# Performance work log

Measured on AMD Instinct MI355X. Metric: run time of the kernel, lower is better.

## Reference

```python
import jax, jax.numpy as jnp
import numpy as np

B, S, H = 64, 512, 768
A1, C1 = 100, 300          # token-attention and sentence-classifier hidden sizes
BETA = 1.0                 # soft_attention_beta
SLW, TLW, RLW = 1.0, 1.0, 0.01  # loss weights


def setup_inputs() -> dict:
    key = jax.random.key(0)
    ks = jax.random.split(key, 12)
    hidden_states = jax.random.normal(ks[0], (B, S, H), jnp.float32)
    # token_attention: Linear(H,100) -> Tanh -> Linear(100,1) -> Sigmoid
    w1 = jax.random.normal(ks[1], (H, A1), jnp.float32) * 0.02
    b1 = jnp.zeros((A1,), jnp.float32)
    w2 = jax.random.normal(ks[2], (A1, 1), jnp.float32) * 0.02
    b2 = jnp.zeros((1,), jnp.float32)
    # sentence_classification: Linear(H,300) -> Tanh -> Linear(300,1) -> Sigmoid
    sw1 = jax.random.normal(ks[3], (H, C1), jnp.float32) * 0.02
    sb1 = jnp.zeros((C1,), jnp.float32)
    sw2 = jax.random.normal(ks[4], (C1, 1), jnp.float32) * 0.02
    sb2 = jnp.zeros((1,), jnp.float32)
    offset_mapping = jax.random.randint(ks[5], (B, S, 2), 0, 4).astype(jnp.int32)
    offset_mapping = offset_mapping.at[:, 0, 0].set(0)  # first token starts a word
    # labels in {-1, 0, 1}; -1 = ignore
    labels = jax.random.randint(ks[6], (B, S), -1, 2).astype(jnp.float32)
    return {
        "hidden_states": hidden_states,
        "w1": w1, "b1": b1, "w2": w2, "b2": b2,
        "sw1": sw1, "sb1": sb1, "sw2": sw2, "sb2": sb2,
        "labels": labels,
        "offset_mapping": offset_mapping,
    }


def _forward(hidden_states, w1, b1, w2, b2, sw1, sb1, sw2, sb2, labels, offset_mapping):
    # token attention scores in (0,1): [B, S]
    token_att = jax.nn.sigmoid(
        jnp.tanh(hidden_states @ w1 + b1) @ w2 + b2
    )[..., 0]

    # ragged per-word subword max-pooling (segment-max along the sequence)
    not_subword = offset_mapping[:, :, 0] == 0                 # [B, S] word starts
    seg = jnp.maximum(jnp.cumsum(not_subword.astype(jnp.int32), axis=1) - 1, 0)

    def _seg_max(vals, seg_ids):
        return jax.ops.segment_max(vals, seg_ids, num_segments=S)

    segmax = jax.vmap(_seg_max)(token_att, seg)                # [B, S] per-word max
    word_att = jnp.where(not_subword, jnp.take_along_axis(segmax, seg, axis=1), 0.0)

    # mask: labeled tokens that are word starts
    token_mask = ((labels != -1) & not_subword).astype(token_att.dtype)
    masked = word_att * token_mask                              # token_logits [B, S]

    # beta-normalized soft attention pooling over hidden states
    p = masked ** BETA
    att_norm = p / jnp.sum(p, axis=1, keepdims=True)            # [B, S]
    pooled = jnp.einsum("bsh,bs->bh", hidden_states, att_norm)  # [B, H]

    sent = jax.nn.sigmoid(jnp.tanh(pooled @ sw1 + sb1) @ sw2 + sb2)  # [B, 1]

    # losses (MSE with reduction='sum')
    sentence_labels = jnp.max(labels, axis=1, keepdims=True)    # [B, 1]
    sentence_loss = jnp.sum((sent - sentence_labels) ** 2)
    zero_labels = jnp.where(labels != -1, labels, 0.0)
    token_loss = jnp.sum((masked - zero_labels) ** 2)
    ones_masked = jnp.where(masked == 0, 1.0, masked)
    reg_a = jnp.sum(jnp.min(ones_masked, axis=1, keepdims=True) ** 2)
    reg_b = jnp.sum((jnp.max(masked, axis=1, keepdims=True) - sentence_labels) ** 2)
    total = SLW * sentence_loss + TLW * token_loss + RLW * (reg_a + reg_b)
    return total, sentence_loss, token_loss, reg_a, reg_b, masked, sent


def reference(hidden_states, w1, b1, w2, b2, sw1, sb1, sw2, sb2, labels, offset_mapping):
    return _forward(hidden_states, w1, b1, w2, b2, sw1, sb1, sw2, sb2,
                    labels, offset_mapping)
```

## Files before the change

### kernel.cpp

```cpp
#include <hip/hip_runtime.h>
#include <math.h>

#define BB 64
#define SS 512
#define HH 768
#define AA1 100
#define CC1 300

typedef __bf16 bf16x8 __attribute__((ext_vector_type(8)));
typedef float f32x4 __attribute__((ext_vector_type(4)));

#ifndef __has_builtin
#define __has_builtin(x) 0
#endif
#if __has_builtin(__builtin_amdgcn_global_load_lds)
#define HAVE_GLL 1
#else
#define HAVE_GLL 0
#endif

#define AS1 __attribute__((address_space(1)))
#define AS3 __attribute__((address_space(3)))

__global__ __launch_bounds__(256) void k_prep(const float* __restrict__ w1,
                                              __bf16* __restrict__ w1i) {
    int idx = blockIdx.x * 256 + threadIdx.x;
    int j = idx % 112;
    int r = idx / 112;
    int e = r & 7, g = r >> 3;
    int k = (g >> 2) * 32 + (g & 3) * 8 + e;
    float v = (j < AA1) ? w1[k * AA1 + j] : 0.f;
    w1i[((size_t)g * 112 + j) * 8 + e] = (__bf16)v;
}

__global__ __launch_bounds__(256) void k_token_att(
        const float* __restrict__ hs, const __bf16* __restrict__ w1i,
        const float* __restrict__ b1, const float* __restrict__ w2,
        const float* __restrict__ b2, float* __restrict__ token_att) {
    __shared__ __attribute__((aligned(16))) float lA[4096];
    __shared__ __attribute__((aligned(16))) __bf16 lB[3584];

    const int tid = threadIdx.x;
    const int tok0 = blockIdx.x * 128;
    const int w = tid >> 6, lane = tid & 63;
    const int q = lane >> 4, ln = lane & 15;
    const int t0 = w * 32 + ln;
    const int t1 = t0 + 16;

    f32x4 acc0[7], acc1[7];
#pragma unroll
    for (int n = 0; n < 7; n++) {
        acc0[n] = (f32x4){0.f, 0.f, 0.f, 0.f};
        acc1[n] = (f32x4){0.f, 0.f, 0.f, 0.f};
    }

    const int p0 = (2 * q) ^ (ln & 7);
    const int p1 = (2 * q + 1) ^ (ln & 7);

    for (int kt = 0; kt < 24; kt++) {
        const int ko = kt * 32;
#pragma unroll
        for (int it = 0; it < 4; it++) {
            int i = tid + it * 256;
            int tt = i >> 3, c = (i & 7) ^ (tt & 7);
            const float* g = hs + (size_t)(tok0 + tt) * HH + ko + c * 4;
#if HAVE_GLL
            __builtin_amdgcn_global_load_lds((AS1 void*)g,
                    (AS3 void*)(lA + (it * 256 + w * 64) * 4), 16, 0, 0);
#else
            *(f32x4*)&lA[i * 4] = *(const f32x4*)g;
#endif
        }
        {
            const __bf16* gb0 = w1i + (size_t)kt * 3584 + (size_t)tid * 8;
#if HAVE_GLL
            __builtin_amdgcn_global_load_lds((AS1 void*)gb0,
                    (AS3 void*)(lB + (w * 64) * 8), 16, 0, 0);
            if (w < 3) {
                const __bf16* gb1 = w1i + (size_t)kt * 3584 + (size_t)(tid + 256) * 8;
                __builtin_amdgcn_global_load_lds((AS1 void*)gb1,
                        (AS3 void*)(lB + (256 + w * 64) * 8), 16, 0, 0);
            }
#else
            *(bf16x8*)&lB[(size_t)tid * 8] = *(const bf16x8*)gb0;
            if (tid < 192) {
                const __bf16* gb1 = w1i + (size_t)kt * 3584 + (size_t)(tid + 256) * 8;
                *(bf16x8*)&lB[(size_t)(tid + 256) * 8] = *(const bf16x8*)gb1;
            }
#endif
        }
        __syncthreads();
        f32x4 a00 = *(f32x4*)&lA[(t0 * 8 + p0) * 4];
        f32x4 a01 = *(f32x4*)&lA[(t0 * 8 + p1) * 4];
        f32x4 a10 = *(f32x4*)&lA[(t1 * 8 + p0) * 4];
        f32x4 a11 = *(f32x4*)&lA[(t1 * 8 + p1) * 4];
        bf16x8 af0, af1;
#pragma unroll
        for (int e = 0; e < 4; e++) {
            af0[e] = (__bf16)a00[e]; af0[e + 4] = (__bf16)a01[e];
            af1[e] = (__bf16)a10[e]; af1[e + 4] = (__bf16)a11[e];
        }
#pragma unroll
        for (int n = 0; n < 7; n++) {
            bf16x8 bf = *(bf16x8*)&lB[((size_t)q * 112 + n * 16 + ln) * 8];
            acc0[n] = __builtin_amdgcn_mfma_f32_16x16x32_bf16(af0, bf, acc0[n], 0, 0, 0);
            acc1[n] = __builtin_amdgcn_mfma_f32_16x16x32_bf16(af1, bf, acc1[n], 0, 0, 0);
        }
        __syncthreads();
    }

    float s0 = 0.f, s1 = 0.f, s2 = 0.f, s3 = 0.f;
    float u0 = 0.f, u1 = 0.f, u2 = 0.f, u3 = 0.f;
#pragma unroll
    for (int n = 0; n < 7; n++) {
        int j = n * 16 + ln;
        if (j < AA1) {
            float bj = b1[j], wj = w2[j];
            s0 += tanhf(acc0[n][0] + bj) * wj;
            s1 += tanhf(acc0[n][1] + bj) * wj;
            s2 += tanhf(acc0[n][2] + bj) * wj;
            s3 += tanhf(acc0[n][3] + bj) * wj;
            u0 += tanhf(acc1[n][0] + bj) * wj;
            u1 += tanhf(acc1[n][1] + bj) * wj;
            u2 += tanhf(acc1[n][2] + bj) * wj;
            u3 += tanhf(acc1[n][3] + bj) * wj;
        }
    }
#pragma unroll
    for (int off = 1; off < 16; off <<= 1) {
        s0 += __shfl_xor(s0, off); s1 += __shfl_xor(s1, off);
        s2 += __shfl_xor(s2, off); s3 += __shfl_xor(s3, off);
        u0 += __shfl_xor(u0, off); u1 += __shfl_xor(u1, off);
        u2 += __shfl_xor(u2, off); u3 += __shfl_xor(u3, off);
    }
    if (ln == 0) {
        float bb = b2[0];
        int base0 = tok0 + w * 32 + q * 4;
        int base1 = base0 + 16;
        token_att[base0 + 0] = 1.f / (1.f + expf(-(s0 + bb)));
        token_att[base0 + 1] = 1.f / (1.f + expf(-(s1 + bb)));
        token_att[base0 + 2] = 1.f / (1.f + expf(-(s2 + bb)));
        token_att[base0 + 3] = 1.f / (1.f + expf(-(s3 + bb)));
        token_att[base1 + 0] = 1.f / (1.f + expf(-(u0 + bb)));
        token_att[base1 + 1] = 1.f / (1.f + expf(-(u1 + bb)));
        token_att[base1 + 2] = 1.f / (1.f + expf(-(u2 + bb)));
        token_att[base1 + 3] = 1.f / (1.f + expf(-(u3 + bb)));
    }
}

__global__ __launch_bounds__(512) void k_mask(
        const float* __restrict__ token_att, const float* __restrict__ labels,
        const int* __restrict__ offm, float* __restrict__ masked_out,
        float* __restrict__ cw_g, short* __restrict__ cs_g,
        int* __restrict__ nnz_g, float* __restrict__ inv_g,
        float4* __restrict__ stats_g, float* __restrict__ out) {
    __shared__ int smax[512];
    __shared__ int wscan[8];
    __shared__ int wscan2[8];
    __shared__ float wred[5][8];

    const int b = blockIdx.x, s = threadIdx.x;
    const int lane = s & 63, wv = s >> 6;
    if (b == 0 && s < 5) out[s] = 0.f;
    const int ns = (offm[(b * SS + s) * 2] == 0) ? 1 : 0;

    int v = ns;
#pragma unroll
    for (int off = 1; off < 64; off <<= 1) {
        int o = __shfl_up(v, off);
        if (lane >= off) v += o;
    }
    if (lane == 63) wscan[wv] = v;
    smax[s] = 0;
    __syncthreads();
    int woff = 0;
    for (int i = 0; i < 8; i++) woff += (i < wv) ? wscan[i] : 0;
    const int seg = max(v + woff - 1, 0);

    const float ta = token_att[b * SS + s];
    atomicMax(&smax[seg], __float_as_int(ta));
    __syncthreads();

    const float wa = ns ? __int_as_float(smax[seg]) : 0.f;
    const float lab = labels[b * SS + s];
    const float m = (lab != -1.f && ns) ? wa : 0.f;
    masked_out[b * SS + s] = m;

    const float zl = (lab != -1.f) ? lab : 0.f;
    const float tl = (m - zl) * (m - zl);
    const float ones = (m == 0.f) ? 1.f : m;

    float r0 = m, r1 = tl, r2 = m, r3 = ones, r4 = lab;
#pragma unroll
    for (int off = 32; off > 0; off >>= 1) {
        r0 += __shfl_xor(r0, off);
        r1 += __shfl_xor(r1, off);
        r2 = fmaxf(r2, __shfl_xor(r2, off));
        r3 = fminf(r3, __shfl_xor(r3, off));
        r4 = fmaxf(r4, __shfl_xor(r4, off));
    }
    if (lane == 0) {
        wred[0][wv] = r0; wred[1][wv] = r1; wred[2][wv] = r2;
        wred[3][wv] = r3; wred[4][wv] = r4;
    }

    const int nz = (m != 0.f) ? 1 : 0;
    int v2 = nz;
#pragma unroll
    for (int off = 1; off < 64; off <<= 1) {
        int o = __shfl_up(v2, off);
        if (lane >= off) v2 += o;
    }
    if (lane == 63) wscan2[wv] = v2;
    __syncthreads();

    int woff2 = 0;
    for (int i = 0; i < 8; i++) woff2 += (i < wv) ? wscan2[i] : 0;
    if (nz) {
        int pos = v2 + woff2 - 1;
        cw_g[b * SS + pos] = m;
        cs_g[b * SS + pos] = (short)s;
    }
    if (s == 0) {
        float att = 0.f, tokl = 0.f, maxm = -1e30f, minone = 1e30f, slab = -1e30f;
        int nnz = 0;
        for (int i = 0; i < 8; i++) {
            att += wred[0][i]; tokl += wred[1][i];
            maxm = fmaxf(maxm, wred[2][i]);
            minone = fminf(minone, wred[3][i]);
            slab = fmaxf(slab, wred[4][i]);
            nnz += wscan2[i];
        }
        nnz_g[b] = nnz;
        inv_g[b] = 1.f / att;
        stats_g[b] = make_float4(tokl, maxm, minone, slab);
    }
}

__global__ __launch_bounds__(512) void k_poolsent(
        const float* __restrict__ hs, const float* __restrict__ cw_g,
        const short* __restrict__ cs_g, const int* __restrict__ nnz_g,
        const float* __restrict__ inv_g, const float4* __restrict__ stats_g,
        const float* __restrict__ sw1, const float* __restrict__ sb1,
        const float* __restrict__ sw2, const float* __restrict__ sb2,
        float* __restrict__ sent_out, float* __restrict__ out) {
    __shared__ float w[SS];
    __shared__ short idx[SS];
    __shared__ float pool[HH];
    __shared__ float wsum[8];

    const int b = blockIdx.x, tid = threadIdx.x;
    const int lane = tid & 63, wv = tid >> 6;
    const int nnz = nnz_g[b];
    if (tid < nnz) { w[tid] = cw_g[b * SS + tid]; idx[tid] = cs_g[b * SS + tid]; }
    __syncthreads();

    const float* hsb = hs + (size_t)b * SS * HH;
    const bool hi = (tid < 256);
    float a[8], c[8];
#pragma unroll
    for (int u = 0; u < 8; u++) { a[u] = 0.f; c[u] = 0.f; }
    int i = 0;
    for (; i + 8 <= nnz; i += 8) {
#pragma unroll
        for (int u = 0; u < 8; u++)
            a[u] += hsb[(size_t)idx[i + u] * HH + tid] * w[i + u];
        if (hi) {
#pragma unroll
            for (int u = 0; u < 8; u++)
                c[u] += hsb[(size_t)idx[i + u] * HH + 512 + tid] * w[i + u];
        }
    }
    for (; i < nnz; i++) {
        a[0] += hsb[(size_t)idx[i] * HH + tid] * w[i];
        if (hi) c[0] += hsb[(size_t)idx[i] * HH + 512 + tid] * w[i];
    }
    const float inv = inv_g[b];
    pool[tid] = (((a[0] + a[1]) + (a[2] + a[3])) + ((a[4] + a[5]) + (a[6] + a[7]))) * inv;
    if (hi)
        pool[512 + tid] = (((c[0] + c[1]) + (c[2] + c[3])) + ((c[4] + c[5]) + (c[6] + c[7]))) * inv;
    __syncthreads();

    float tt = 0.f;
    if (tid < CC1) {
        float z = sb1[tid];
#pragma unroll 8
        for (int k = 0; k < HH; k++) z += pool[k] * sw1[k * CC1 + tid];
        tt = tanhf(z) * sw2[tid];
    }
#pragma unroll
    for (int off = 32; off > 0; off >>= 1) tt += __shfl_xor(tt, off);
    if (lane == 0) wsum[wv] = tt;
    __syncthreads();
    if (tid == 0) {
        float zsum = wsum[0] + wsum[1] + wsum[2] + wsum[3] + wsum[4];
        float sv = 1.f / (1.f + expf(-(zsum + sb2[0])));
        sent_out[b] = sv;
        float4 st = stats_g[b];
        float vs = sv - st.w; vs *= vs;
        float ra = st.z * st.z;
        float rb = st.y - st.w; rb *= rb;
        atomicAdd(&out[1], vs);
        atomicAdd(&out[2], st.x);
        atomicAdd(&out[3], ra);
        atomicAdd(&out[4], rb);
        atomicAdd(&out[0], vs + st.x + 0.01f * (ra + rb));
    }
}

extern "C" void kernel_launch(void* const* d_in, const int* in_sizes, int n_in,
                              void* d_out, int out_size, void* d_ws, size_t ws_size,
                              hipStream_t stream) {
    const float* hs  = (const float*)d_in[0];
    const float* w1  = (const float*)d_in[1];
    const float* b1  = (const float*)d_in[2];
    const float* w2  = (const float*)d_in[3];
    const float* b2  = (const float*)d_in[4];
    const float* sw1 = (const float*)d_in[5];
    const float* sb1 = (const float*)d_in[6];
    const float* sw2 = (const float*)d_in[7];
    const float* sb2 = (const float*)d_in[8];
    const float* labels = (const float*)d_in[9];
    const int*   offm   = (const int*)d_in[10];

    float* out = (float*)d_out;
    float* ws  = (float*)d_ws;

    float*  token_att = ws;
    __bf16* w1i    = (__bf16*)(ws + 32768);
    float*  cw     = ws + 32768 + 43008;
    short*  cs     = (short*)(cw + 32768);
    int*    nnz    = (int*)(cw + 32768 + 16384);
    float*  inv    = (float*)(nnz + 64);
    float4* stats  = (float4*)(inv + 64);

    float* masked_out = out + 5;
    float* sent_out   = out + 5 + BB * SS;

    hipLaunchKernelGGL(k_prep, dim3(336), dim3(256), 0, stream, w1, w1i);
    hipLaunchKernelGGL(k_token_att, dim3(256), dim3(256), 0, stream,
                       hs, w1i, b1, w2, b2, token_att);
    hipLaunchKernelGGL(k_mask, dim3(BB), dim3(512), 0, stream,
                       token_att, labels, offm, masked_out,
                       cw, cs, nnz, inv, stats, out);
    hipLaunchKernelGGL(k_poolsent, dim3(BB), dim3(512), 0, stream,
                       hs, cw, cs, nnz, inv, stats,
                       sw1, sb1, sw2, sb2, sent_out, out);
}
```

Before: 246.6 us.

## Load GEMM operands directly to registers and split pooling across more blocks

The token-attention GEMM drops its LDS staging and barriers: each lane now reads its A and B fragments straight from global memory into registers. The weighted pooling, which ran as one 512-thread block per batch row, is split into 8 blocks per row that accumulate into a zeroed pooled buffer with atomics. A separate small kernel then applies the sentence classifier. This adds one kernel launch and float atomics, which make the reduction order nondeterministic. The direct loads may also be less coalesced, since each lane reads 32-byte strips spread across rows.

Result: no change. 248.3 us (+0.7%).

```diff
diff --git a/kernel.cpp b/kernel.cpp
--- a/kernel.cpp
+++ b/kernel.cpp
@@ -9,18 +9,6 @@
 
 typedef __bf16 bf16x8 __attribute__((ext_vector_type(8)));
 typedef float f32x4 __attribute__((ext_vector_type(4)));
-
-#ifndef __has_builtin
-#define __has_builtin(x) 0
-#endif
-#if __has_builtin(__builtin_amdgcn_global_load_lds)
-#define HAVE_GLL 1
-#else
-#define HAVE_GLL 0
-#endif
-
-#define AS1 __attribute__((address_space(1)))
-#define AS3 __attribute__((address_space(3)))
 
 __global__ __launch_bounds__(256) void k_prep(const float* __restrict__ w1,
                                               __bf16* __restrict__ w1i) {
@@ -37,15 +25,14 @@
         const float* __restrict__ hs, const __bf16* __restrict__ w1i,
         const float* __restrict__ b1, const float* __restrict__ w2,
         const float* __restrict__ b2, float* __restrict__ token_att) {
-    __shared__ __attribute__((aligned(16))) float lA[4096];
-    __shared__ __attribute__((aligned(16))) __bf16 lB[3584];
-
     const int tid = threadIdx.x;
     const int tok0 = blockIdx.x * 128;
     const int w = tid >> 6, lane = tid & 63;
     const int q = lane >> 4, ln = lane & 15;
-    const int t0 = w * 32 + ln;
-    const int t1 = t0 + 16;
+
+    const float* pa0 = hs + (size_t)(tok0 + w * 32 + ln) * HH + q * 8;
+    const float* pa1 = pa0 + (size_t)16 * HH;
+    const __bf16* pb = w1i + ((size_t)q * 112 + ln) * 8;
 
     f32x4 acc0[7], acc1[7];
 #pragma unroll
@@ -54,46 +41,16 @@
         acc1[n] = (f32x4){0.f, 0.f, 0.f, 0.f};
     }
 
-    const int p0 = (2 * q) ^ (ln & 7);
-    const int p1 = (2 * q + 1) ^ (ln & 7);
-
+#pragma unroll 2
     for (int kt = 0; kt < 24; kt++) {
-        const int ko = kt * 32;
-#pragma unroll
-        for (int it = 0; it < 4; it++) {
-            int i = tid + it * 256;
-            int tt = i >> 3, c = (i & 7) ^ (tt & 7);
-            const float* g = hs + (size_t)(tok0 + tt) * HH + ko + c * 4;
-#if HAVE_GLL
-            __builtin_amdgcn_global_load_lds((AS1 void*)g,
-                    (AS3 void*)(lA + (it * 256 + w * 64) * 4), 16, 0, 0);
-#else
-            *(f32x4*)&lA[i * 4] = *(const f32x4*)g;
-#endif
-        }
-        {
-            const __bf16* gb0 = w1i + (size_t)kt * 3584 + (size_t)tid * 8;
-#if HAVE_GLL
-            __builtin_amdgcn_global_load_lds((AS1 void*)gb0,
-                    (AS3 void*)(lB + (w * 64) * 8), 16, 0, 0);
-            if (w < 3) {
-                const __bf16* gb1 = w1i + (size_t)kt * 3584 + (size_t)(tid + 256) * 8;
-                __builtin_amdgcn_global_load_lds((AS1 void*)gb1,
-                        (AS3 void*)(lB + (256 + w * 64) * 8), 16, 0, 0);
-            }
-#else
-            *(bf16x8*)&lB[(size_t)tid * 8] = *(const bf16x8*)gb0;
-            if (tid < 192) {
-                const __bf16* gb1 = w1i + (size_t)kt * 3584 + (size_t)(tid + 256) * 8;
-                *(bf16x8*)&lB[(size_t)(tid + 256) * 8] = *(const bf16x8*)gb1;
-            }
-#endif
-        }
-        __syncthreads();
-        f32x4 a00 = *(f32x4*)&lA[(t0 * 8 + p0) * 4];
-        f32x4 a01 = *(f32x4*)&lA[(t0 * 8 + p1) * 4];
-        f32x4 a10 = *(f32x4*)&lA[(t1 * 8 + p0) * 4];
-        f32x4 a11 = *(f32x4*)&lA[(t1 * 8 + p1) * 4];
+        f32x4 a00 = *(const f32x4*)(pa0 + kt * 32);
+        f32x4 a01 = *(const f32x4*)(pa0 + kt * 32 + 4);
+        f32x4 a10 = *(const f32x4*)(pa1 + kt * 32);
+        f32x4 a11 = *(const f32x4*)(pa1 + kt * 32 + 4);
+        bf16x8 bfr[7];
+#pragma unroll
+        for (int n = 0; n < 7; n++)
+            bfr[n] = *(const bf16x8*)(pb + (size_t)kt * 3584 + n * 128);
         bf16x8 af0, af1;
 #pragma unroll
         for (int e = 0; e < 4; e++) {
@@ -102,11 +59,9 @@
         }
 #pragma unroll
         for (int n = 0; n < 7; n++) {
-            bf16x8 bf = *(bf16x8*)&lB[((size_t)q * 112 + n * 16 + ln) * 8];
-            acc0[n] = __builtin_amdgcn_mfma_f32_16x16x32_bf16(af0, bf, acc0[n], 0, 0, 0);
-            acc1[n] = __builtin_amdgcn_mfma_f32_16x16x32_bf16(af1, bf, acc1[n], 0, 0, 0);
+            acc0[n] = __builtin_amdgcn_mfma_f32_16x16x32_bf16(af0, bfr[n], acc0[n], 0, 0, 0);
+            acc1[n] = __builtin_amdgcn_mfma_f32_16x16x32_bf16(af1, bfr[n], acc1[n], 0, 0, 0);
         }
-        __syncthreads();
     }
 
     float s0 = 0.f, s1 = 0.f, s2 = 0.f, s3 = 0.f;
@@ -153,7 +108,8 @@
         const int* __restrict__ offm, float* __restrict__ masked_out,
         float* __restrict__ cw_g, short* __restrict__ cs_g,
         int* __restrict__ nnz_g, float* __restrict__ inv_g,
-        float4* __restrict__ stats_g, float* __restrict__ out) {
+        float4* __restrict__ stats_g, float* __restrict__ pooled,
+        float* __restrict__ out) {
     __shared__ int smax[512];
     __shared__ int wscan[8];
     __shared__ int wscan2[8];
@@ -162,6 +118,8 @@
     const int b = blockIdx.x, s = threadIdx.x;
     const int lane = s & 63, wv = s >> 6;
     if (b == 0 && s < 5) out[s] = 0.f;
+    pooled[b * HH + s] = 0.f;
+    if (s < HH - SS) pooled[b * HH + SS + s] = 0.f;
     const int ns = (offm[(b * SS + s) * 2] == 0) ? 1 : 0;
 
     int v = ns;
@@ -237,55 +195,47 @@
     }
 }
 
-__global__ __launch_bounds__(512) void k_poolsent(
+__global__ __launch_bounds__(256) void k_pool(
         const float* __restrict__ hs, const float* __restrict__ cw_g,
         const short* __restrict__ cs_g, const int* __restrict__ nnz_g,
-        const float* __restrict__ inv_g, const float4* __restrict__ stats_g,
+        float* __restrict__ pooled) {
+    const int b = blockIdx.x, g = blockIdx.y, tid = threadIdx.x;
+    const int nnz = nnz_g[b];
+    const float* hsb = hs + (size_t)b * SS * HH;
+    float a0 = 0.f, a1 = 0.f, a2 = 0.f;
+#pragma unroll 2
+    for (int i = g; i < nnz; i += 8) {
+        const float wv = cw_g[b * SS + i];
+        const int s = cs_g[b * SS + i];
+        const float* hp = hsb + (size_t)s * HH;
+        a0 += hp[tid] * wv;
+        a1 += hp[tid + 256] * wv;
+        a2 += hp[tid + 512] * wv;
+    }
+    atomicAdd(&pooled[b * HH + tid], a0);
+    atomicAdd(&pooled[b * HH + tid + 256], a1);
+    atomicAdd(&pooled[b * HH + tid + 512], a2);
+}
+
+__global__ __launch_bounds__(320) void k_sentfinal(
+        const float* __restrict__ pooled, const float* __restrict__ inv_g,
+        const float4* __restrict__ stats_g,
         const float* __restrict__ sw1, const float* __restrict__ sb1,
         const float* __restrict__ sw2, const float* __restrict__ sb2,
         float* __restrict__ sent_out, float* __restrict__ out) {
-    __shared__ float w[SS];
-    __shared__ short idx[SS];
-    __shared__ float pool[HH];
-    __shared__ float wsum[8];
-
+    __shared__ float p[HH];
+    __shared__ float wsum[5];
     const int b = blockIdx.x, tid = threadIdx.x;
     const int lane = tid & 63, wv = tid >> 6;
-    const int nnz = nnz_g[b];
-    if (tid < nnz) { w[tid] = cw_g[b * SS + tid]; idx[tid] = cs_g[b * SS + tid]; }
-    __syncthreads();
-
-    const float* hsb = hs + (size_t)b * SS * HH;
-    const bool hi = (tid < 256);
-    float a[8], c[8];
-#pragma unroll
-    for (int u = 0; u < 8; u++) { a[u] = 0.f; c[u] = 0.f; }
-    int i = 0;
-    for (; i + 8 <= nnz; i += 8) {
-#pragma unroll
-        for (int u = 0; u < 8; u++)
-            a[u] += hsb[(size_t)idx[i + u] * HH + tid] * w[i + u];
-        if (hi) {
-#pragma unroll
-            for (int u = 0; u < 8; u++)
-                c[u] += hsb[(size_t)idx[i + u] * HH + 512 + tid] * w[i + u];
-        }
-    }
-    for (; i < nnz; i++) {
-        a[0] += hsb[(size_t)idx[i] * HH + tid] * w[i];
-        if (hi) c[0] += hsb[(size_t)idx[i] * HH + 512 + tid] * w[i];
-    }
     const float inv = inv_g[b];
-    pool[tid] = (((a[0] + a[1]) + (a[2] + a[3])) + ((a[4] + a[5]) + (a[6] + a[7]))) * inv;
-    if (hi)
-        pool[512 + tid] = (((c[0] + c[1]) + (c[2] + c[3])) + ((c[4] + c[5]) + (c[6] + c[7]))) * inv;
+    for (int i = tid; i < HH; i += 320) p[i] = pooled[b * HH + i] * inv;
     __syncthreads();
 
     float tt = 0.f;
     if (tid < CC1) {
         float z = sb1[tid];
 #pragma unroll 8
-        for (int k = 0; k < HH; k++) z += pool[k] * sw1[k * CC1 + tid];
+        for (int k = 0; k < HH; k++) z += p[k] * sw1[k * CC1 + tid];
         tt = tanhf(z) * sw2[tid];
     }
 #pragma unroll
@@ -333,6 +283,7 @@
     int*    nnz    = (int*)(cw + 32768 + 16384);
     float*  inv    = (float*)(nnz + 64);
     float4* stats  = (float4*)(inv + 64);
+    float*  pooled = inv + 64 + 256;
 
     float* masked_out = out + 5;
     float* sent_out   = out + 5 + BB * SS;
@@ -342,8 +293,9 @@
                        hs, w1i, b1, w2, b2, token_att);
     hipLaunchKernelGGL(k_mask, dim3(BB), dim3(512), 0, stream,
                        token_att, labels, offm, masked_out,
-                       cw, cs, nnz, inv, stats, out);
-    hipLaunchKernelGGL(k_poolsent, dim3(BB), dim3(512), 0, stream,
-                       hs, cw, cs, nnz, inv, stats,
-                       sw1, sb1, sw2, sb2, sent_out, out);
-}
+                       cw, cs, nnz, inv, stats, pooled, out);
+    hipLaunchKernelGGL(k_pool, dim3(BB, 8), dim3(256), 0, stream,
+                       hs, cw, cs, nnz, pooled);
+    hipLaunchKernelGGL(k_sentfinal, dim3(BB), dim3(320), 0, stream,
+                       pooled, inv, stats, sw1, sb1, sw2, sb2, sent_out, out);
+}
```
